# Kernel tuning notes

Measured on AMD Instinct MI355X. Metric: run time of the kernel, lower is better.

## Reference

```python
import jax, jax.numpy as jnp
import numpy as np

K_DIFF = 2  # max_diffusion_step


def _gconv(x, supports, W, b):
    # x: (B, N, D) node features; diffusion convolution with Chebyshev-style recurrence
    mats = [x]
    for S in supports:
        x0 = x
        x1 = jnp.einsum('mn,bnd->bmd', S, x)
        mats.append(x1)
        for _ in range(2, K_DIFF + 1):
            x2 = 2.0 * jnp.einsum('mn,bnd->bmd', S, x1) - x0
            mats.append(x2)
            x0, x1 = x1, x2
    xcat = jnp.concatenate(mats, axis=-1)  # (B, N, num_matrices*D)
    return xcat @ W + b


def _dcgru_layer(seq, h0, supports, Wg, bg, Wc, bc):
    # seq: (T, B, N, D); h0: (B, N, H)
    def step(h, xt):
        ru = jax.nn.sigmoid(_gconv(jnp.concatenate([xt, h], -1), supports, Wg, bg))
        r, u = jnp.split(ru, 2, axis=-1)
        c = jnp.tanh(_gconv(jnp.concatenate([xt, r * h], -1), supports, Wc, bc))
        hn = u * h + (1.0 - u) * c
        return hn, hn
    _, out = jax.lax.scan(step, h0, seq)
    return out  # (T, B, N, H)


def setup_inputs():
    key = jax.random.key(0)
    ks = jax.random.split(key, 10)
    B, T, N, D, H, C = 32, 128, 64, 64, 64, 4
    num_mat = 2 * K_DIFF + 1
    input_seq = jax.random.normal(ks[0], (B, T, N, D), jnp.float32)
    seq_lengths = jax.random.randint(ks[1], (B,), 1, T + 1)
    A = jax.random.uniform(ks[2], (N, N), jnp.float32)
    support0 = A / A.sum(axis=1, keepdims=True)        # forward random walk
    support1 = A.T / A.T.sum(axis=1, keepdims=True)    # reverse random walk
    w = lambda k, s: jax.random.normal(k, s, jnp.float32) * 0.05
    Wg0 = w(ks[3], ((D + H) * num_mat, 2 * H)); bg0 = jnp.ones((2 * H,), jnp.float32)
    Wc0 = w(ks[4], ((D + H) * num_mat, H));     bc0 = jnp.zeros((H,), jnp.float32)
    Wg1 = w(ks[5], ((H + H) * num_mat, 2 * H)); bg1 = jnp.ones((2 * H,), jnp.float32)
    Wc1 = w(ks[6], ((H + H) * num_mat, H));     bc1 = jnp.zeros((H,), jnp.float32)
    Wp = w(ks[7], (H, C)); bp = jnp.zeros((C,), jnp.float32)
    return dict(input_seq=input_seq, seq_lengths=seq_lengths, support0=support0,
                support1=support1, Wg0=Wg0, bg0=bg0, Wc0=Wc0, bc0=bc0,
                Wg1=Wg1, bg1=bg1, Wc1=Wc1, bc1=bc1, Wp=Wp, bp=bp)


def reference(input_seq, seq_lengths, support0, support1,
              Wg0, bg0, Wc0, bc0, Wg1, bg1, Wc1, bc1, Wp, bp):
    B, T, N, D = input_seq.shape
    H = Wc0.shape[1]
    supports = (support0, support1)
    seq = jnp.transpose(input_seq, (1, 0, 2, 3))  # (T, B, N, D)
    h0 = jnp.zeros((B, N, H), input_seq.dtype)
    out0 = _dcgru_layer(seq, h0, supports, Wg0, bg0, Wc0, bc0)   # (T,B,N,H)
    out1 = _dcgru_layer(out0, h0, supports, Wg1, bg1, Wc1, bc1)  # (T,B,N,H)
    idx = jnp.clip(seq_lengths - 1, 0, T - 1)
    last = out1[idx, jnp.arange(B)]               # (B, N, H) last relevant timestep
    logits = jax.nn.relu(last) @ Wp + bp          # (B, N, C); dropout is identity (eval)
    return jnp.max(logits, axis=1)                # max-pool over nodes -> (B, C)
```

## Files before the change

### kernel.cpp

```cpp
#include <hip/hip_runtime.h>
#include <stdint.h>


typedef short short8 __attribute__((ext_vector_type(8)));
typedef float float4v __attribute__((ext_vector_type(4)));
typedef unsigned short ushort4v __attribute__((ext_vector_type(4)));
typedef unsigned int uint4v __attribute__((ext_vector_type(4)));
typedef unsigned int uint2v __attribute__((ext_vector_type(2)));

#define MF(a,b,c) __builtin_amdgcn_mfma_f32_16x16x32_bf16(a,b,c,0,0,0)

__device__ __forceinline__ unsigned short f2bf(float v){
  unsigned int x = __builtin_bit_cast(unsigned int, v);
  x += 0x7FFFu + ((x >> 16) & 1u);
  return (unsigned short)(x >> 16);
}
__device__ __forceinline__ float bf2f(unsigned short h){
  unsigned int x = ((unsigned int)h) << 16;
  return __builtin_bit_cast(float, x);
}
__device__ __forceinline__ void cvt_hilo(const float4v v, ushort4v& oh, ushort4v& ol){
#pragma unroll
  for (int r=0;r<4;r++){ unsigned short h=f2bf(v[r]); oh[r]=h; ol[r]=f2bf(v[r]-bf2f(h)); }
}

__device__ __forceinline__ unsigned int cvtpk(float a, float b){
  unsigned int r;
  asm("v_cvt_pk_bf16_f32 %0, %1, %2" : "=v"(r) : "v"(a), "v"(b));
  return r;
}
__device__ __forceinline__ float bcf(unsigned int x){
  return __builtin_bit_cast(float, x);
}
__device__ __forceinline__ void cvt_hilo_pk(const float4v v,
    unsigned int& h0, unsigned int& h1, unsigned int& l0, unsigned int& l1){
  h0 = cvtpk(v[0], v[1]);
  h1 = cvtpk(v[2], v[3]);
  l0 = cvtpk(v[0]-bcf(h0<<16), v[1]-bcf(h0&0xffff0000u));
  l1 = cvtpk(v[2]-bcf(h1<<16), v[3]-bcf(h1&0xffff0000u));
}

#define PLO 4608
#define XP  0
#define HP  9216
#define RH  18432
#define YS0 27648
#define YS1 36864
#define YS2 46080
#define YS3 55296
#define Z0F 32256
#define Z1F 36608
#define LDS_BYTES 163840

#define WSF_S2   16384
#define WSF_WG0  32768
#define WSF_WC0  196608
#define WSF_WG1  278528
#define WSF_WC1  442368
#define WSF_CAP  524288
#define WSF_FLAG 655360
#define WSF_DONE 663552
#define WSF_SLOT 663616
#define WSF_SQS  4857920

#define TB(grp,j,nt) ((((grp)*5+(j))*4+(nt))*4)

__device__ __forceinline__ void store_Y(unsigned short* lds_, int buf, int nt,
                                        int fc, int qd, const float4v* acc){
#pragma unroll
  for (int Mt=0;Mt<4;Mt++){
    unsigned int h0,h1,l0,l1;
    cvt_hilo_pk(acc[Mt],h0,h1,l0,l1);
    const int o = buf + (16*nt+fc)*72 + 16*Mt + 4*qd;
    uint2v hv; hv[0]=h0; hv[1]=h1;
    uint2v lv; lv[0]=l0; lv[1]=l1;
    *(uint2v*)(lds_+o)=hv; *(uint2v*)(lds_+o+PLO)=lv;
  }
}

__device__ __forceinline__ void p1_group(unsigned short* lds_,
    const unsigned short* __restrict__ wfr, int grp, int p0, int p1,
    float bias, float4v* gacc, int w, int ln, int fc, int qd)
{
  const int nt = w & 3;
  const bool lo = (w < 4);
  float4v aY0[4], aY1[4];
#pragma unroll
  for (int Mt=0;Mt<4;Mt++){
    aY0[Mt]=(float4v){0.f,0.f,0.f,0.f};
    aY1[Mt]=(float4v){0.f,0.f,0.f,0.f};
  }
#pragma unroll
  for (int i=0;i<2;i++) gacc[i]=(float4v){bias,bias,bias,bias};
  const int tbG = TB(grp,0,nt);
  const int tbA = lo ? TB(grp,1,nt) : TB(grp,2,nt);
  const int tbB = lo ? TB(grp,3,nt) : TB(grp,4,nt);
#pragma unroll
  for (int kt=0;kt<4;kt++){
    const int pb = (kt<2)? p0 : p1;
    short8 ah[4], al[4];
#pragma unroll
    for (int Mt=0;Mt<4;Mt++){
      const int o = pb + (16*Mt+fc)*72 + 32*(kt&1) + 8*qd;
      ah[Mt]=*(const short8*)(lds_+o);
      al[Mt]=*(const short8*)(lds_+o+PLO);
    }
    {
      const unsigned short* wb = wfr + (size_t)((tbG+kt)*2)*512 + ln*8;
      short8 bh=*(const short8*)wb, bl=*(const short8*)(wb+512);
      if (lo){
        gacc[0]=MF(ah[0],bh,gacc[0]); gacc[0]=MF(ah[0],bl,gacc[0]);
        gacc[0]=MF(al[0],bh,gacc[0]);
        gacc[1]=MF(ah[1],bh,gacc[1]); gacc[1]=MF(ah[1],bl,gacc[1]);
        gacc[1]=MF(al[1],bh,gacc[1]);
      } else {
        gacc[0]=MF(ah[2],bh,gacc[0]); gacc[0]=MF(ah[2],bl,gacc[0]);
        gacc[0]=MF(al[2],bh,gacc[0]);
        gacc[1]=MF(ah[3],bh,gacc[1]); gacc[1]=MF(ah[3],bl,gacc[1]);
        gacc[1]=MF(al[3],bh,gacc[1]);
      }
    }
    {
      const unsigned short* wb = wfr + (size_t)((tbA+kt)*2)*512 + ln*8;
      short8 bh=*(const short8*)wb, bl=*(const short8*)(wb+512);
#pragma unroll
      for (int Mt=0;Mt<4;Mt++){
        aY0[Mt]=MF(ah[Mt],bh,aY0[Mt]); aY0[Mt]=MF(ah[Mt],bl,aY0[Mt]);
        aY0[Mt]=MF(al[Mt],bh,aY0[Mt]);
      }
    }
    {
      const unsigned short* wb = wfr + (size_t)((tbB+kt)*2)*512 + ln*8;
      short8 bh=*(const short8*)wb, bl=*(const short8*)(wb+512);
#pragma unroll
      for (int Mt=0;Mt<4;Mt++){
        aY1[Mt]=MF(ah[Mt],bh,aY1[Mt]); aY1[Mt]=MF(ah[Mt],bl,aY1[Mt]);
        aY1[Mt]=MF(al[Mt],bh,aY1[Mt]);
      }
    }
  }
  store_Y(lds_, lo? YS0 : YS1, nt, fc, qd, aY0);
  store_Y(lds_, lo? YS2 : YS3, nt, fc, qd, aY1);
}

__device__ __forceinline__ void p2_fused(unsigned short* lds_,
    const short8* sfA, const short8* sfB, int sup, int mt, int fc, int qd)
{
  const int ya = sup? YS2 : YS0;
  const int yb = sup? YS3 : YS1;
  float* zf = (float*)lds_ + (sup? Z1F : Z0F);
#pragma unroll
  for (int nt=0;nt<4;nt++){
    float4v acc = {0.f,0.f,0.f,0.f};
#pragma unroll
    for (int kt=0;kt<2;kt++){
      {
        const int bo = ya + (16*nt+fc)*72 + 32*kt + 8*qd;
        short8 bh=*(const short8*)(lds_+bo), bl=*(const short8*)(lds_+bo+PLO);
        acc=MF(sfA[kt*2+0],bh,acc); acc=MF(sfA[kt*2+0],bl,acc); acc=MF(sfA[kt*2+1],bh,acc);
      }
      {
        const int bo = yb + (16*nt+fc)*72 + 32*kt + 8*qd;
        short8 bh=*(const short8*)(lds_+bo), bl=*(const short8*)(lds_+bo+PLO);
        acc=MF(sfB[kt*2+0],bh,acc); acc=MF(sfB[kt*2+0],bl,acc); acc=MF(sfB[kt*2+1],bh,acc);
      }
    }
    *(float4v*)(zf + (16*nt+fc)*68 + 16*mt + 4*qd) = acc;
  }
}

__device__ __forceinline__ void read_pre(const unsigned short* lds_,
    const float4v* gacc, float4v* pre, int mo, int ntg, int fc, int qd)
{
  const float* lf = (const float*)lds_;
#pragma unroll
  for (int i=0;i<2;i++){
    const int Mt = mo+i;
    float4v za = *(const float4v*)(lf + Z0F + (16*ntg+fc)*68 + 16*Mt + 4*qd);
    float4v zb = *(const float4v*)(lf + Z1F + (16*ntg+fc)*68 + 16*Mt + 4*qd);
    pre[i] = gacc[i] + za + zb;
  }
}

__device__ __forceinline__ void scatter_plane(unsigned short* lds_, int plane,
    int mo, int ntg, int fc, int qd, const ushort4v* oh, const ushort4v* ol)
{
#pragma unroll
  for (int i=0;i<2;i++){
#pragma unroll
    for (int r=0;r<4;r++){
      const int o = plane + (16*(mo+i)+4*qd+r)*72 + 16*ntg+fc;
      lds_[o] = oh[i][r]; lds_[o+PLO] = ol[i][r];
    }
  }
}

__global__ void __launch_bounds__(512, 2)
dcrnn_main(const float* __restrict__ input_seq, const int* __restrict__ seq_lengths,
           const float* __restrict__ bg0, const float* __restrict__ bc0,
           const float* __restrict__ bg1, const float* __restrict__ bc1,
           const float* __restrict__ Wp, const float* __restrict__ bp,
           unsigned short* __restrict__ ws, float* __restrict__ out)
{
  extern __shared__ unsigned short lds_[];
  const int tid = threadIdx.x;
  const int w = tid>>6, ln = tid&63, fc = ln&15, qd = ln>>4;
  const int role = blockIdx.x >> 5;
  const int b = blockIdx.x & 31;

  const unsigned short* frags = ws;
  int* flags = (int*)(ws + WSF_FLAG) + b*128;
  int* done  = (int*)(ws + WSF_DONE) + b;
  unsigned short* capb = ws + WSF_CAP + (size_t)b*4096;
  unsigned int* slots = (unsigned int*)(ws + WSF_SLOT);

  { unsigned int* l32 = (unsigned int*)lds_;
    for (int i=4608+tid; i<9216; i+=512) l32[i]=0u; }

  const int sup = (w>>2)&1, mt = w&3;
  short8 sfA[4], sfB[4];
#pragma unroll
  for (int kt=0;kt<2;kt++)
#pragma unroll
    for (int pl=0;pl<2;pl++){
      const size_t o = (size_t)((((sup*2+pl)*4+mt)*2+kt)*512 + ln*8);
      sfA[kt*2+pl] = *(const short8*)(frags + o);
      sfB[kt*2+pl] = *(const short8*)(frags + WSF_S2 + o);
    }

  const bool lo = (w < 4);
  const int mo = lo ? 0 : 2, ntg = w & 3;
  const int gcol = 16*ntg + fc;

  const unsigned short* WGf = frags + (role? WSF_WG1 : WSF_WG0);
  const unsigned short* WCf = frags + (role? WSF_WC1 : WSF_WC0);
  const float* bg = role? bg1 : bg0;
  const float* bc = role? bc1 : bc0;
  const float brv = bg[gcol];
  const float buv = bg[64+gcol];
  const float bcv = bc[gcol];

  int tl = 0;
  if (role){ tl = seq_lengths[b]-1; tl = tl<0?0:(tl>127?127:tl); }

  float4v h_old[2], uv[2], gaccR[2], gaccU[2], gaccC[2];
#pragma unroll
  for (int i=0;i<2;i++) h_old[i]=(float4v){0.f,0.f,0.f,0.f};
  __syncthreads();

#pragma unroll 1
  for (int t=0; t<128; ++t){
    if (role==0){
      if (t>=16 && tid==0){
        while ((int)__hip_atomic_load(done, __ATOMIC_ACQUIRE, __HIP_MEMORY_SCOPE_AGENT) < t-15)
          __builtin_amdgcn_s_sleep(1);
      }
      const int node = tid>>3, f0 = (tid&7)*8;
      const float* src = input_seq + (((size_t)b*128 + t)*64 + node)*64 + f0;
      float4v v0 = *(const float4v*)(src);
      float4v v1 = *(const float4v*)(src+4);
      unsigned int h0,h1,h2,h3, l0,l1,l2,l3;
      cvt_hilo_pk(v0, h0,h1, l0,l1);
      cvt_hilo_pk(v1, h2,h3, l2,l3);
      uint4v hv; hv[0]=h0; hv[1]=h1; hv[2]=h2; hv[3]=h3;
      uint4v lv; lv[0]=l0; lv[1]=l1; lv[2]=l2; lv[3]=l3;
      *(uint4v*)(lds_ + XP + node*72 + f0) = hv;
      *(uint4v*)(lds_ + XP + PLO + node*72 + f0) = lv;
      __syncthreads();
    } else {
      if (tid==0){
        while (__hip_atomic_load(&flags[t], __ATOMIC_ACQUIRE, __HIP_MEMORY_SCOPE_AGENT) != t+1)
          __builtin_amdgcn_s_sleep(1);
        __threadfence();
      }
      __syncthreads();
      {
        const unsigned int* sl = slots + ((size_t)(b*16 + (t&15)))*4096 + (w*64+ln)*8;
#pragma unroll
        for (int i=0;i<2;i++){
          uint4v v = *(const uint4v*)(sl + i*4);
#pragma unroll
          for (int r=0;r<4;r++){
            const int o = XP + (16*(mo+i)+4*qd+r)*72 + gcol;
            lds_[o] = (unsigned short)(v[r] & 0xffffu);
            lds_[o+PLO] = (unsigned short)(v[r] >> 16);
          }
        }
      }
      __syncthreads();
      if (tid==0)
        __hip_atomic_store(done, t+1, __ATOMIC_RELEASE, __HIP_MEMORY_SCOPE_AGENT);
    }

    p1_group(lds_, WGf, 0, XP, HP, brv, gaccR, w, ln, fc, qd);
    __syncthreads();
    p2_fused(lds_, sfA, sfB, sup, mt, fc, qd);
    __syncthreads();

    p1_group(lds_, WGf, 1, XP, HP, buv, gaccU, w, ln, fc, qd);
    {
      float4v pre[2]; read_pre(lds_, gaccR, pre, mo, ntg, fc, qd);
      ushort4v oh[2], ol[2];
#pragma unroll
      for (int i=0;i<2;i++){
        float4v rh;
#pragma unroll
        for (int r=0;r<4;r++){
          float rv = 1.f/(1.f+__expf(-pre[i][r]));
          rh[r] = rv*h_old[i][r];
        }
        unsigned int h0,h1,l0,l1;
        cvt_hilo_pk(rh, h0,h1, l0,l1);
        oh[i][0]=(unsigned short)h0; oh[i][1]=(unsigned short)(h0>>16);
        oh[i][2]=(unsigned short)h1; oh[i][3]=(unsigned short)(h1>>16);
        ol[i][0]=(unsigned short)l0; ol[i][1]=(unsigned short)(l0>>16);
        ol[i][2]=(unsigned short)l1; ol[i][3]=(unsigned short)(l1>>16);
      }
      scatter_plane(lds_, RH, mo, ntg, fc, qd, oh, ol);
    }
    __syncthreads();
    p2_fused(lds_, sfA, sfB, sup, mt, fc, qd);
    __syncthreads();

    p1_group(lds_, WCf, 0, XP, RH, bcv, gaccC, w, ln, fc, qd);
    {
      float4v pre[2]; read_pre(lds_, gaccU, pre, mo, ntg, fc, qd);
#pragma unroll
      for (int i=0;i<2;i++)
#pragma unroll
        for (int r=0;r<4;r++) uv[i][r] = 1.f/(1.f+__expf(-pre[i][r]));
    }
    __syncthreads();
    p2_fused(lds_, sfA, sfB, sup, mt, fc, qd);
    __syncthreads();

    {
      float4v pre[2]; read_pre(lds_, gaccC, pre, mo, ntg, fc, qd);
      ushort4v oh[2], ol[2];
#pragma unroll
      for (int i=0;i<2;i++){
        float4v hn;
#pragma unroll
        for (int r=0;r<4;r++){
          float x = fminf(pre[i][r], 15.f);
          float e = __expf(2.f*x);
          float cv = (e-1.f)/(e+1.f);
          float u1 = uv[i][r];
          hn[r] = u1*h_old[i][r] + (1.f-u1)*cv;
        }
        h_old[i] = hn;
        cvt_hilo(hn, oh[i], ol[i]);
      }
      scatter_plane(lds_, HP, mo, ntg, fc, qd, oh, ol);
      if (role==0){
        unsigned int* sl = slots + ((size_t)(b*16 + (t&15)))*4096 + (w*64+ln)*8;
#pragma unroll
        for (int i=0;i<2;i++){
          uint4v pk;
#pragma unroll
          for (int r=0;r<4;r++)
            pk[r] = (unsigned int)oh[i][r] | ((unsigned int)ol[i][r] << 16);
          *(uint4v*)(sl + i*4) = pk;
        }
      } else if (t==tl){
#pragma unroll
        for (int i=0;i<2;i++)
#pragma unroll
          for (int r=0;r<4;r++)
            capb[(16*(mo+i)+4*qd+r)*64 + gcol] = oh[i][r];
      }
    }
    __syncthreads();
    if (role==0 && tid==0){
      __threadfence();
      __hip_atomic_store(&flags[t], t+1, __ATOMIC_RELEASE, __HIP_MEMORY_SCOPE_AGENT);
    }
  }

  if (role==0) return;

  __threadfence();
  __syncthreads();
  float* sc = (float*)lds_;
  if (tid < 64){
    const unsigned short* hpx = capb + tid*64;
    float4v acc = {bp[0], bp[1], bp[2], bp[3]};
#pragma unroll 1
    for (int ch = 0; ch < 64; ++ch){
      float h = fmaxf(bf2f(hpx[ch]), 0.f);
      const float4v wr = *(const float4v*)(Wp + ch*4);
      acc += h * wr;
    }
    sc[tid*4+0]=acc[0]; sc[tid*4+1]=acc[1]; sc[tid*4+2]=acc[2]; sc[tid*4+3]=acc[3];
  }
  __syncthreads();
  if (tid < 4){
    float m = sc[tid];
#pragma unroll 1
    for (int n=1;n<64;n++) m = fmaxf(m, sc[n*4 + tid]);
    out[b*4 + tid] = m;
  }
}

__global__ void __launch_bounds__(256)
dcrnn_sq(const float* __restrict__ S0, const float* __restrict__ S1,
         float* __restrict__ sqs)
{
  const float* S = blockIdx.x ? S1 : S0;
  float* D = sqs + blockIdx.x*4096;
  const int i = threadIdx.x >> 2, j0 = (threadIdx.x & 3)*16;
  float acc[16];
#pragma unroll
  for (int j=0;j<16;j++) acc[j]=0.f;
#pragma unroll 4
  for (int k=0;k<64;k++){
    float s = S[i*64+k];
    const float* row = S + k*64 + j0;
#pragma unroll
    for (int j=0;j<16;j++) acc[j] += s*row[j];
  }
#pragma unroll
  for (int j=0;j<16;j++) D[i*64+j0+j]=acc[j];
}

__global__ void __launch_bounds__(256)
dcrnn_prep(const float* __restrict__ S0, const float* __restrict__ S1,
           const float* __restrict__ Wg0, const float* __restrict__ Wc0,
           const float* __restrict__ Wg1, const float* __restrict__ Wc1,
           const float* __restrict__ sqs, unsigned short* __restrict__ frags)
{
  const int uid = blockIdx.x*256 + threadIdx.x;
  if (uid >= 65536) return;
  short8 o;
  unsigned short* dst;
  if (uid < 4096){
    int r = uid & 2047;
    const bool issq = uid >= 2048;
    const int lane = r & 63; r >>= 6;
    const int kt = r & 1; r >>= 1;
    const int Mt = r & 3; r >>= 2;
    const int pl = r & 1; r >>= 1;
    const float* S = issq ? (sqs + r*4096) : (r ? S1 : S0);
    const int m  = 16*Mt + (lane & 15);
    const int k0 = 32*kt + 8*(lane >> 4);
#pragma unroll
    for (int j=0;j<8;j++){
      float v = S[m*64 + k0 + j];
      unsigned short hi = f2bf(v);
      o[j] = (short)(pl ? f2bf(v - bf2f(hi)) : hi);
    }
    dst = frags + (issq ? WSF_S2 : 0) + (size_t)(uid & 2047)*8;
  } else {
    int u2 = uid - 4096;
    const float* W; int wld; size_t base;
    if      (u2 < 20480){ W = Wg0; wld = 128; base = WSF_WG0; }
    else if (u2 < 30720){ W = Wc0; wld = 64;  base = WSF_WC0; u2 -= 20480; }
    else if (u2 < 51200){ W = Wg1; wld = 128; base = WSF_WG1; u2 -= 30720; }
    else                { W = Wc1; wld = 64;  base = WSF_WC1; u2 -= 51200; }
    const int lane = u2 & 63;
    const int pl   = (u2 >> 6) & 1;
    const int rest = u2 >> 7;
    const int kt = rest & 3;
    const int nt = (rest >> 2) & 3;
    const int j  = (rest >> 4) % 5;
    const int grp= (rest >> 4) / 5;
    const int col = grp*64 + 16*nt + (lane & 15);
    const int k0  = 32*kt + 8*(lane >> 4);
#pragma unroll
    for (int jj=0;jj<8;jj++){
      const int k = k0 + jj;
      float v;
      if (j == 0)
        v = W[(size_t)k*wld + col] - W[(size_t)(256+k)*wld + col] - W[(size_t)(512+k)*wld + col];
      else {
        v = W[(size_t)(j*128 + k)*wld + col];
        if (j == 2 || j == 4) v *= 2.f;
      }
      unsigned short hi = f2bf(v);
      o[jj] = (short)(pl ? f2bf(v - bf2f(hi)) : hi);
    }
    dst = frags + base + (size_t)u2*8;
  }
  *(short8*)dst = o;
}

extern "C" void kernel_launch(void* const* d_in, const int* in_sizes, int n_in,
                              void* d_out, int out_size, void* d_ws, size_t ws_size,
                              hipStream_t stream) {
  const float* input_seq   = (const float*)d_in[0];
  const int*   seq_lengths = (const int*)  d_in[1];
  const float* S0  = (const float*)d_in[2];
  const float* S1  = (const float*)d_in[3];
  const float* Wg0 = (const float*)d_in[4];
  const float* bg0 = (const float*)d_in[5];
  const float* Wc0 = (const float*)d_in[6];
  const float* bc0 = (const float*)d_in[7];
  const float* Wg1 = (const float*)d_in[8];
  const float* bg1 = (const float*)d_in[9];
  const float* Wc1 = (const float*)d_in[10];
  const float* bc1 = (const float*)d_in[11];
  const float* Wp  = (const float*)d_in[12];
  const float* bp  = (const float*)d_in[13];

  unsigned short* ws = (unsigned short*)d_ws;
  float* sqs = (float*)(ws + WSF_SQS);

  dcrnn_sq<<<dim3(2), dim3(256), 0, stream>>>(S0, S1, sqs);
  dcrnn_prep<<<dim3(256), dim3(256), 0, stream>>>(S0, S1, Wg0, Wc0, Wg1, Wc1, sqs, ws);

  (void)hipFuncSetAttribute((const void*)dcrnn_main,
                            hipFuncAttributeMaxDynamicSharedMemorySize, LDS_BYTES);
  dcrnn_main<<<dim3(64), dim3(512), LDS_BYTES, stream>>>(
      input_seq, seq_lengths, bg0, bc0, bg1, bc1, Wp, bp, ws, (float*)d_out);
}
```

Before: 2.507 ms.

## Prefetch next-step inputs and overlap inter-layer handoff with final diffusion phase

Layer-0 blocks now load the input for step t+2 from global memory during the candidate phase and write step t+1's XP plane to LDS during the last diffusion pass. Layer-1 blocks wait for the producer flag and fetch the next slot during that same phase. This removes the load, wait and barrier at the top of each timestep, taking global-load latency and spin-wait time off the serial recurrence. The cost is extra registers and more intricate flag/done ordering, and it relies on the last diffusion pass not reading the XP region being overwritten.

Result: faster. 2.441 ms (median of 3 runs) (-2.6%).

```diff
diff --git a/kernel.cpp b/kernel.cpp
--- a/kernel.cpp
+++ b/kernel.cpp
@@ -76,6 +76,17 @@
     uint2v lv; lv[0]=l0; lv[1]=l1;
     *(uint2v*)(lds_+o)=hv; *(uint2v*)(lds_+o+PLO)=lv;
   }
+}
+
+__device__ __forceinline__ void xp_write_pk(unsigned short* lds_, int node, int f0,
+                                            float4v a0, float4v a1){
+  unsigned int h0,h1,h2,h3, l0,l1,l2,l3;
+  cvt_hilo_pk(a0, h0,h1, l0,l1);
+  cvt_hilo_pk(a1, h2,h3, l2,l3);
+  uint4v hv; hv[0]=h0; hv[1]=h1; hv[2]=h2; hv[3]=h3;
+  uint4v lv; lv[0]=l0; lv[1]=l1; lv[2]=l2; lv[3]=l3;
+  *(uint4v*)(lds_ + XP + node*72 + f0) = hv;
+  *(uint4v*)(lds_ + XP + PLO + node*72 + f0) = lv;
 }
 
 __device__ __forceinline__ void p1_group(unsigned short* lds_,
@@ -246,52 +257,46 @@
   float4v h_old[2], uv[2], gaccR[2], gaccU[2], gaccC[2];
 #pragma unroll
   for (int i=0;i<2;i++) h_old[i]=(float4v){0.f,0.f,0.f,0.f};
+
+  const int node8 = tid>>3, f08 = (tid&7)*8;
+  float4v v_nxt0 = {0.f,0.f,0.f,0.f}, v_nxt1 = {0.f,0.f,0.f,0.f};
   __syncthreads();
+
+  if (role==0){
+    const float* s0 = input_seq + (((size_t)b*128 + 0)*64 + node8)*64 + f08;
+    float4v a0 = *(const float4v*)(s0);
+    float4v a1 = *(const float4v*)(s0+4);
+    xp_write_pk(lds_, node8, f08, a0, a1);
+    const float* s1 = input_seq + (((size_t)b*128 + 1)*64 + node8)*64 + f08;
+    v_nxt0 = *(const float4v*)(s1); v_nxt1 = *(const float4v*)(s1+4);
+    __syncthreads();
+  } else {
+    if (tid==0){
+      while (__hip_atomic_load(&flags[0], __ATOMIC_ACQUIRE, __HIP_MEMORY_SCOPE_AGENT) != 1)
+        __builtin_amdgcn_s_sleep(1);
+      __threadfence();
+    }
+    __syncthreads();
+    {
+      const unsigned int* sl = slots + ((size_t)(b*16 + 0))*4096 + (w*64+ln)*8;
+#pragma unroll
+      for (int i=0;i<2;i++){
+        uint4v v = *(const uint4v*)(sl + i*4);
+#pragma unroll
+        for (int r=0;r<4;r++){
+          const int o = XP + (16*(mo+i)+4*qd+r)*72 + gcol;
+          lds_[o] = (unsigned short)(v[r] & 0xffffu);
+          lds_[o+PLO] = (unsigned short)(v[r] >> 16);
+        }
+      }
+    }
+    __syncthreads();
+    if (tid==0)
+      __hip_atomic_store(done, 1, __ATOMIC_RELEASE, __HIP_MEMORY_SCOPE_AGENT);
+  }
 
 #pragma unroll 1
   for (int t=0; t<128; ++t){
-    if (role==0){
-      if (t>=16 && tid==0){
-        while ((int)__hip_atomic_load(done, __ATOMIC_ACQUIRE, __HIP_MEMORY_SCOPE_AGENT) < t-15)
-          __builtin_amdgcn_s_sleep(1);
-      }
-      const int node = tid>>3, f0 = (tid&7)*8;
-      const float* src = input_seq + (((size_t)b*128 + t)*64 + node)*64 + f0;
-      float4v v0 = *(const float4v*)(src);
-      float4v v1 = *(const float4v*)(src+4);
-      unsigned int h0,h1,h2,h3, l0,l1,l2,l3;
-      cvt_hilo_pk(v0, h0,h1, l0,l1);
-      cvt_hilo_pk(v1, h2,h3, l2,l3);
-      uint4v hv; hv[0]=h0; hv[1]=h1; hv[2]=h2; hv[3]=h3;
-      uint4v lv; lv[0]=l0; lv[1]=l1; lv[2]=l2; lv[3]=l3;
-      *(uint4v*)(lds_ + XP + node*72 + f0) = hv;
-      *(uint4v*)(lds_ + XP + PLO + node*72 + f0) = lv;
-      __syncthreads();
-    } else {
-      if (tid==0){
-        while (__hip_atomic_load(&flags[t], __ATOMIC_ACQUIRE, __HIP_MEMORY_SCOPE_AGENT) != t+1)
-          __builtin_amdgcn_s_sleep(1);
-        __threadfence();
-      }
-      __syncthreads();
-      {
-        const unsigned int* sl = slots + ((size_t)(b*16 + (t&15)))*4096 + (w*64+ln)*8;
-#pragma unroll
-        for (int i=0;i<2;i++){
-          uint4v v = *(const uint4v*)(sl + i*4);
-#pragma unroll
-          for (int r=0;r<4;r++){
-            const int o = XP + (16*(mo+i)+4*qd+r)*72 + gcol;
-            lds_[o] = (unsigned short)(v[r] & 0xffffu);
-            lds_[o+PLO] = (unsigned short)(v[r] >> 16);
-          }
-        }
-      }
-      __syncthreads();
-      if (tid==0)
-        __hip_atomic_store(done, t+1, __ATOMIC_RELEASE, __HIP_MEMORY_SCOPE_AGENT);
-    }
-
     p1_group(lds_, WGf, 0, XP, HP, brv, gaccR, w, ln, fc, qd);
     __syncthreads();
     p2_fused(lds_, sfA, sfB, sup, mt, fc, qd);
@@ -331,10 +336,36 @@
         for (int r=0;r<4;r++) uv[i][r] = 1.f/(1.f+__expf(-pre[i][r]));
     }
     __syncthreads();
-    p2_fused(lds_, sfA, sfB, sup, mt, fc, qd);
-    __syncthreads();
-
-    {
+
+    if (role==0){
+      if (t<127) xp_write_pk(lds_, node8, f08, v_nxt0, v_nxt1);
+      p2_fused(lds_, sfA, sfB, sup, mt, fc, qd);
+      if (tid==0 && t>=16){
+        while ((int)__hip_atomic_load(done, __ATOMIC_ACQUIRE, __HIP_MEMORY_SCOPE_AGENT) < t-15)
+          __builtin_amdgcn_s_sleep(1);
+      }
+    } else {
+      p2_fused(lds_, sfA, sfB, sup, mt, fc, qd);
+      if (tid==0 && t<127){
+        while (__hip_atomic_load(&flags[t+1], __ATOMIC_ACQUIRE, __HIP_MEMORY_SCOPE_AGENT) != t+2)
+          __builtin_amdgcn_s_sleep(1);
+        __threadfence();
+      }
+    }
+    __syncthreads();
+
+    {
+      uint4v sv0, sv1;
+      sv0[0]=0;sv0[1]=0;sv0[2]=0;sv0[3]=0; sv1=sv0;
+      if (role && t<127){
+        const unsigned int* sl = slots + ((size_t)(b*16 + ((t+1)&15)))*4096 + (w*64+ln)*8;
+        sv0 = *(const uint4v*)(sl);
+        sv1 = *(const uint4v*)(sl + 4);
+      }
+      if (role==0 && t<126){
+        const float* s2 = input_seq + (((size_t)b*128 + (t+2))*64 + node8)*64 + f08;
+        v_nxt0 = *(const float4v*)(s2); v_nxt1 = *(const float4v*)(s2+4);
+      }
       float4v pre[2]; read_pre(lds_, gaccC, pre, mo, ntg, fc, qd);
       ushort4v oh[2], ol[2];
 #pragma unroll
@@ -362,18 +393,36 @@
             pk[r] = (unsigned int)oh[i][r] | ((unsigned int)ol[i][r] << 16);
           *(uint4v*)(sl + i*4) = pk;
         }
-      } else if (t==tl){
-#pragma unroll
-        for (int i=0;i<2;i++)
-#pragma unroll
-          for (int r=0;r<4;r++)
-            capb[(16*(mo+i)+4*qd+r)*64 + gcol] = oh[i][r];
-      }
-    }
-    __syncthreads();
-    if (role==0 && tid==0){
-      __threadfence();
-      __hip_atomic_store(&flags[t], t+1, __ATOMIC_RELEASE, __HIP_MEMORY_SCOPE_AGENT);
+      } else {
+        if (t==tl){
+#pragma unroll
+          for (int i=0;i<2;i++)
+#pragma unroll
+            for (int r=0;r<4;r++)
+              capb[(16*(mo+i)+4*qd+r)*64 + gcol] = oh[i][r];
+        }
+        if (t<127){
+#pragma unroll
+          for (int i=0;i<2;i++){
+            uint4v v = i ? sv1 : sv0;
+#pragma unroll
+            for (int r=0;r<4;r++){
+              const int o = XP + (16*(mo+i)+4*qd+r)*72 + gcol;
+              lds_[o] = (unsigned short)(v[r] & 0xffffu);
+              lds_[o+PLO] = (unsigned short)(v[r] >> 16);
+            }
+          }
+        }
+      }
+    }
+    __syncthreads();
+    if (tid==0){
+      if (role==0){
+        __threadfence();
+        __hip_atomic_store(&flags[t], t+1, __ATOMIC_RELEASE, __HIP_MEMORY_SCOPE_AGENT);
+      } else if (t<127){
+        __hip_atomic_store(done, t+2, __ATOMIC_RELEASE, __HIP_MEMORY_SCOPE_AGENT);
+      }
     }
   }
 
```
